# Kernel optimization log

Hardware: AMD Instinct MI355X
Metric: run time of the kernel (lower is better)

Reference implementation:

```python
import jax, jax.numpy as jnp
import numpy as np

B, T, D_MODEL, NHEAD, D_HEAD = 8, 4096, 1024, 16, 64


def setup_inputs() -> dict:
    key = jax.random.key(0)
    ks = jax.random.split(key, 8)
    return {
        "inputs": jax.random.normal(ks[0], (B, T, D_MODEL), jnp.float32),
        "z0": jax.random.normal(ks[1], (NHEAD, D_HEAD), jnp.float32),
        "W_in": jax.random.normal(ks[2], (D_MODEL, D_MODEL), jnp.float32) / np.sqrt(D_MODEL),
        "b_in": jax.random.normal(ks[3], (D_MODEL,), jnp.float32) * 0.01,
        "W_out": jax.random.normal(ks[4], (D_MODEL, D_MODEL), jnp.float32) / np.sqrt(D_MODEL),
        "b_out": jax.random.normal(ks[5], (D_MODEL,), jnp.float32) * 0.01,
        "smoothing_logit": jax.random.normal(ks[6], (NHEAD, 1), jnp.float32),
        "v0": jax.random.normal(ks[7], (1, 1, NHEAD, D_HEAD), jnp.float32),
    }


def reference(inputs, z0, W_in, b_in, W_out, b_out, smoothing_logit, v0):
    b, t, d = inputs.shape
    nhead, d_head = z0.shape
    # in projection -> (b, t, h, d_head)
    values = (inputs @ W_in + b_in).reshape(b, t, nhead, d_head)
    # prepend learned z0, then temporal differencing -> (b, t, h, d_head)
    z0_b = jnp.broadcast_to(z0[None, None], (b, 1, nhead, d_head))
    values = jnp.concatenate([z0_b, values], axis=1)
    values = values[:, 1:] - values[:, :-1]
    # exponential smoothing recurrence: s_j = a*s_{j-1} + (1-a)*v_j, s_{-1} = v0
    alpha = jax.nn.sigmoid(smoothing_logit)           # (h, 1)
    a = alpha[None]                                   # (1, h, 1) broadcast over batch
    s0 = jnp.broadcast_to(v0[0, 0][None], (b, nhead, d_head))

    def step(s, v):                                   # v: (b, h, d_head)
        s = a * s + (1.0 - a) * v
        return s, s

    _, es_out = jax.lax.scan(step, s0, jnp.swapaxes(values, 0, 1))  # (t, b, h, d)
    es_out = jnp.swapaxes(es_out, 0, 1)               # (b, t, h, d_head)
    # prepend v0 -> length t+1
    v0_b = jnp.broadcast_to(v0, (b, 1, nhead, d_head))
    out = jnp.concatenate([v0_b, es_out], axis=1)     # (b, t+1, h, d_head)
    out = out.reshape(b, t + 1, nhead * d_head)
    return out @ W_out + b_out                        # (b, t+1, d_model)
```

## Files before the change

### kernel.cpp

```cpp
#include <hip/hip_runtime.h>
#include <hip/hip_bf16.h>
#include <stdint.h>

#define DEV static __device__ __forceinline__

typedef __attribute__((ext_vector_type(8))) short bf16x8;
typedef __attribute__((ext_vector_type(4))) float f32x4;
typedef unsigned int u32;

static constexpr int T = 4096;
static constexpr int BATCH = 8;
static constexpr int DM = 1024;
static constexpr int M1 = BATCH * T;
static constexpr int M2 = BATCH * (T + 1);
static constexpr int M2P = 257 * 128;
static constexpr int NCH = 64;
static constexpr int CL = T / NCH;

DEV unsigned short f2bf(float f) {
  union { float f; unsigned u; } v; v.f = f;
  unsigned u = v.u;
  return (unsigned short)((u + 0x7fffu + ((u >> 16) & 1u)) >> 16);
}
DEV float bf2f(unsigned short s) {
  union { unsigned u; float f; } v; v.u = ((unsigned)s) << 16;
  return v.f;
}

DEV void gl_lds16(const unsigned short* g, unsigned short* lds) {
  __builtin_amdgcn_global_load_lds(
      (const __attribute__((address_space(1))) u32*)g,
      (__attribute__((address_space(3))) u32*)lds,
      16, 0, 0);
}

__global__ void k_cvt_x(const float4* __restrict__ x, ushort4* __restrict__ o) {
  int i = blockIdx.x * 256 + threadIdx.x;
  float4 v = x[i];
  ushort4 r;
  r.x = f2bf(v.x); r.y = f2bf(v.y); r.z = f2bf(v.z); r.w = f2bf(v.w);
  o[i] = r;
}

__global__ void k_transpose(const float* __restrict__ w0, const float* __restrict__ w1,
                            unsigned short* __restrict__ t0, unsigned short* __restrict__ t1) {
  __shared__ float tile[32][33];
  const float* src = blockIdx.z ? w1 : w0;
  unsigned short* dst = blockIdx.z ? t1 : t0;
  int bx = blockIdx.x * 32;
  int by = blockIdx.y * 32;
  int tx = threadIdx.x & 31, ty = threadIdx.x >> 5;
#pragma unroll
  for (int r = 0; r < 32; r += 8)
    tile[ty + r][tx] = src[(by + ty + r) * DM + bx + tx];
  __syncthreads();
#pragma unroll
  for (int r = 0; r < 32; r += 8)
    dst[(bx + ty + r) * DM + by + tx] = f2bf(tile[tx][ty + r]);
}

template <int MODE>
__global__ __launch_bounds__(256) void k_gemm(const unsigned short* __restrict__ A16,
                                              const unsigned short* __restrict__ Bt16,
                                              const float* __restrict__ bias,
                                              unsigned short* __restrict__ outb,
                                              float* __restrict__ outf, int Mvalid) {
  __shared__ unsigned short sA[128 * 32];
  __shared__ unsigned short sB[128 * 32];

  const int tid = threadIdx.x;
  const int w = tid >> 6, l = tid & 63;

  const int nwg = gridDim.x;
  const int cpx = nwg >> 3;
  const int orig = blockIdx.x;
  const int wg = (orig & 7) * cpx + (orig >> 3);
  const int bm = wg >> 3, bn = wg & 7;
  const int blockM = bm * 128;
  const int blockN = bn * 128;
  const int wr = (w >> 1) * 64, wc = (w & 1) * 64;

  f32x4 acc[4][4];
#pragma unroll
  for (int m = 0; m < 4; m++)
#pragma unroll
    for (int n = 0; n < 4; n++) acc[m][n] = (f32x4){0.f, 0.f, 0.f, 0.f};

  const int srow0 = tid >> 2;
  const int sslot = tid & 3;

  auto stage = [&](int kt) {
    const int k0 = kt * 32;
#pragma unroll
    for (int c = 0; c < 2; c++) {
      const int row = c * 64 + srow0;
      const unsigned short* gA = A16 + (size_t)(blockM + row) * DM + k0 + sslot * 8;
      const unsigned short* gB = Bt16 + (size_t)(blockN + row) * DM + k0 + sslot * 8;
      unsigned short* lA = sA + c * 2048 + w * 512;
      unsigned short* lB = sB + c * 2048 + w * 512;
      gl_lds16(gA, lA);
      gl_lds16(gB, lB);
    }
  };

  const int kg = l >> 4;
  const int rr = l & 15;

  stage(0);
  __syncthreads();

  for (int kt = 0; kt < 32; ++kt) {
    bf16x8 af[4], bfr[4];
#pragma unroll
    for (int m = 0; m < 4; m++)
      af[m] = *(const bf16x8*)(sA + (wr + m * 16 + rr) * 32 + kg * 8);
#pragma unroll
    for (int n = 0; n < 4; n++)
      bfr[n] = *(const bf16x8*)(sB + (wc + n * 16 + rr) * 32 + kg * 8);
#pragma unroll
    for (int m = 0; m < 4; m++)
#pragma unroll
      for (int n = 0; n < 4; n++)
        acc[m][n] = __builtin_amdgcn_mfma_f32_16x16x32_bf16(af[m], bfr[n], acc[m][n], 0, 0, 0);
    __syncthreads();
    if (kt + 1 < 32) {
      stage(kt + 1);
      __syncthreads();
    }
  }

#pragma unroll
  for (int m = 0; m < 4; m++) {
    int row = blockM + wr + m * 16 + (l >> 4) * 4;
#pragma unroll
    for (int n = 0; n < 4; n++) {
      int col = blockN + wc + n * 16 + (l & 15);
      float bv = bias[col];
#pragma unroll
      for (int j = 0; j < 4; j++) {
        float v = acc[m][n][j] + bv;
        if (MODE == 0) {
          outb[(size_t)(row + j) * DM + col] = f2bf(v);
        } else {
          if (row + j < Mvalid) outf[(size_t)(row + j) * DM + col] = v;
        }
      }
    }
  }
}

__global__ void k_scan_partial(const unsigned short* __restrict__ proj,
                               const float* __restrict__ logit,
                               const float* __restrict__ z0,
                               float* __restrict__ chunkend) {
  int b = blockIdx.x >> 6, c = blockIdx.x & 63;
  int ch = threadIdx.x;
  float a = 1.f / (1.f + expf(-logit[ch >> 6]));
  int t0 = c * CL;
  const unsigned short* p = proj + (size_t)(b * T + t0) * DM + ch;
  float pprev = (t0 == 0) ? z0[ch] : bf2f(p[-DM]);
  float s = 0.f;
  for (int j = 0; j < CL; j++) {
    float pv = bf2f(p[(size_t)j * DM]);
    s = a * s + (1.f - a) * (pv - pprev);
    pprev = pv;
  }
  chunkend[(b * NCH + c) * DM + ch] = s;
}

__global__ void k_scan_combine(const float* __restrict__ chunkend,
                               const float* __restrict__ logit,
                               const float* __restrict__ v0,
                               float* __restrict__ enter) {
  int b = blockIdx.x;
  int ch = threadIdx.x;
  float a = 1.f / (1.f + expf(-logit[ch >> 6]));
  float a2 = a * a, a4 = a2 * a2, a8 = a4 * a4, a16 = a8 * a8, a32 = a16 * a16;
  float aL = a32 * a32;
  float e = v0[ch];
  enter[(b * NCH + 0) * DM + ch] = e;
  for (int c = 1; c < NCH; c++) {
    e = aL * e + chunkend[(b * NCH + c - 1) * DM + ch];
    enter[(b * NCH + c) * DM + ch] = e;
  }
}

__global__ void k_scan_final(const unsigned short* __restrict__ proj,
                             const float* __restrict__ logit,
                             const float* __restrict__ z0,
                             const float* __restrict__ v0,
                             const float* __restrict__ enter,
                             unsigned short* __restrict__ S) {
  int b = blockIdx.x >> 6, c = blockIdx.x & 63;
  int ch = threadIdx.x;
  float a = 1.f / (1.f + expf(-logit[ch >> 6]));
  int t0 = c * CL;
  const unsigned short* p = proj + (size_t)(b * T + t0) * DM + ch;
  unsigned short* so = S + (size_t)(b * (T + 1) + t0 + 1) * DM + ch;
  float pprev = (t0 == 0) ? z0[ch] : bf2f(p[-DM]);
  float s = enter[(b * NCH + c) * DM + ch];
  if (c == 0) S[(size_t)b * (T + 1) * DM + ch] = f2bf(v0[ch]);
  for (int j = 0; j < CL; j++) {
    float pv = bf2f(p[(size_t)j * DM]);
    s = a * s + (1.f - a) * (pv - pprev);
    pprev = pv;
    so[(size_t)j * DM] = f2bf(s);
  }
}

__global__ void k_pad(unsigned short* __restrict__ S) {
  int i = blockIdx.x * 256 + threadIdx.x;
  S[(size_t)M2 * DM + i] = 0;
}

extern "C" void kernel_launch(void* const* d_in, const int* in_sizes, int n_in,
                              void* d_out, int out_size, void* d_ws, size_t ws_size,
                              hipStream_t stream) {
  const float* inputs = (const float*)d_in[0];
  const float* z0     = (const float*)d_in[1];
  const float* W_in   = (const float*)d_in[2];
  const float* b_in   = (const float*)d_in[3];
  const float* W_out  = (const float*)d_in[4];
  const float* b_out  = (const float*)d_in[5];
  const float* slogit = (const float*)d_in[6];
  const float* v0     = (const float*)d_in[7];
  float* out = (float*)d_out;

  char* ws = (char*)d_ws;
  unsigned short* X16   = (unsigned short*)(ws);
  unsigned short* P16   = (unsigned short*)(ws + 67108864);
  unsigned short* S16   = (unsigned short*)(ws + 134217728);
  unsigned short* WTin  = (unsigned short*)(ws + 201588736);
  unsigned short* WTout = (unsigned short*)(ws + 203685888);
  float* chunkend       = (float*)(ws + 205783040);
  float* enter          = (float*)(ws + 207880192);

  k_cvt_x<<<32768, 256, 0, stream>>>((const float4*)inputs, (ushort4*)X16);
  k_transpose<<<dim3(32, 32, 2), 256, 0, stream>>>(W_in, W_out, WTin, WTout);
  k_gemm<0><<<dim3((M1 / 128) * 8), 256, 0, stream>>>(X16, WTin, b_in, P16, nullptr, M1);
  k_scan_partial<<<dim3(BATCH * NCH), 1024, 0, stream>>>(P16, slogit, z0, chunkend);
  k_scan_combine<<<dim3(BATCH), 1024, 0, stream>>>(chunkend, slogit, v0, enter);
  k_scan_final<<<dim3(BATCH * NCH), 1024, 0, stream>>>(P16, slogit, z0, v0, enter, S16);
  k_pad<<<dim3(480), 256, 0, stream>>>(S16);
  k_gemm<1><<<dim3((M2P / 128) * 8), 256, 0, stream>>>(S16, WTout, b_out, nullptr, out, M2);
}
```

Before: 315.3 us.

## Rewrite GEMM with 256x256 tiles, 4-stage async LDS pipeline and swizzle

```diff
diff --git a/kernel.cpp b/kernel.cpp
--- a/kernel.cpp
+++ b/kernel.cpp
@@ -13,9 +13,10 @@
 static constexpr int DM = 1024;
 static constexpr int M1 = BATCH * T;
 static constexpr int M2 = BATCH * (T + 1);
-static constexpr int M2P = 257 * 128;
+static constexpr int M2P = 129 * 256;
 static constexpr int NCH = 64;
 static constexpr int CL = T / NCH;
+static constexpr int NT = 32;
 
 DEV unsigned short f2bf(float f) {
   union { float f; unsigned u; } v; v.f = f;
@@ -60,85 +61,116 @@
 }
 
 template <int MODE>
-__global__ __launch_bounds__(256) void k_gemm(const unsigned short* __restrict__ A16,
-                                              const unsigned short* __restrict__ Bt16,
-                                              const float* __restrict__ bias,
-                                              unsigned short* __restrict__ outb,
-                                              float* __restrict__ outf, int Mvalid) {
-  __shared__ unsigned short sA[128 * 32];
-  __shared__ unsigned short sB[128 * 32];
+__global__ __launch_bounds__(512, 2) void k_gemm(const unsigned short* __restrict__ A16,
+                                                 const unsigned short* __restrict__ Bt16,
+                                                 const float* __restrict__ bias,
+                                                 unsigned short* __restrict__ outb,
+                                                 float* __restrict__ outf, int Mvalid) {
+  __shared__ unsigned short lds[4 * 16384];
 
   const int tid = threadIdx.x;
   const int w = tid >> 6, l = tid & 63;
-
-  const int nwg = gridDim.x;
-  const int cpx = nwg >> 3;
-  const int orig = blockIdx.x;
-  const int wg = (orig & 7) * cpx + (orig >> 3);
-  const int bm = wg >> 3, bn = wg & 7;
-  const int blockM = bm * 128;
-  const int blockN = bn * 128;
-  const int wr = (w >> 1) * 64, wc = (w & 1) * 64;
-
-  f32x4 acc[4][4];
-#pragma unroll
-  for (int m = 0; m < 4; m++)
+  const int wm = w >> 2, wn = w & 3;
+  const int rr = l & 15, kg = l >> 4;
+
+  const int nwg = gridDim.x, orig = blockIdx.x;
+  const int q = nwg >> 3, r8 = nwg & 7;
+  const int xcd = orig & 7, idx = orig >> 3;
+  const int wg = (xcd < r8 ? xcd * (q + 1) : r8 * (q + 1) + (xcd - r8) * q) + idx;
+  const int bm = wg >> 2, bn = wg & 3;
+  const int blockM = bm * 256;
+  const int blockN = bn * 256;
+
+  f32x4 acc[8][4];
+#pragma unroll
+  for (int m = 0; m < 8; m++)
 #pragma unroll
     for (int n = 0; n < 4; n++) acc[m][n] = (f32x4){0.f, 0.f, 0.f, 0.f};
 
-  const int srow0 = tid >> 2;
-  const int sslot = tid & 3;
-
-  auto stage = [&](int kt) {
-    const int k0 = kt * 32;
-#pragma unroll
-    for (int c = 0; c < 2; c++) {
-      const int row = c * 64 + srow0;
-      const unsigned short* gA = A16 + (size_t)(blockM + row) * DM + k0 + sslot * 8;
-      const unsigned short* gB = Bt16 + (size_t)(blockN + row) * DM + k0 + sslot * 8;
-      unsigned short* lA = sA + c * 2048 + w * 512;
-      unsigned short* lB = sB + c * 2048 + w * 512;
-      gl_lds16(gA, lA);
-      gl_lds16(gB, lB);
-    }
+  const unsigned short* pA[2];
+  const unsigned short* pB[2];
+#pragma unroll
+  for (int cc = 0; cc < 2; cc++) {
+    int rp = w * 32 + cc * 16 + (l >> 2);
+    int sl = (l & 3) ^ ((rp >> 1) & 3);
+    pA[cc] = A16 + (size_t)(blockM + rp) * DM + sl * 8;
+    pB[cc] = Bt16 + (size_t)(blockN + rp) * DM + sl * 8;
+  }
+
+  int offA[8], offB[4];
+#pragma unroll
+  for (int mf = 0; mf < 8; mf++) {
+    int rrow = wm * 128 + mf * 16 + rr;
+    offA[mf] = rrow * 32 + ((kg ^ ((rrow >> 1) & 3)) * 8);
+  }
+#pragma unroll
+  for (int nf = 0; nf < 4; nf++) {
+    int rb = wn * 64 + nf * 16 + rr;
+    offB[nf] = 8192 + rb * 32 + ((kg ^ ((rb >> 1) & 3)) * 8);
+  }
+
+  auto stageA = [&](int t) {
+    unsigned short* d = lds + (t & 3) * 16384 + w * 1024;
+#pragma unroll
+    for (int cc = 0; cc < 2; cc++) gl_lds16(pA[cc] + (size_t)t * 32, d + cc * 512);
   };
-
-  const int kg = l >> 4;
-  const int rr = l & 15;
-
-  stage(0);
-  __syncthreads();
-
-  for (int kt = 0; kt < 32; ++kt) {
-    bf16x8 af[4], bfr[4];
-#pragma unroll
-    for (int m = 0; m < 4; m++)
-      af[m] = *(const bf16x8*)(sA + (wr + m * 16 + rr) * 32 + kg * 8);
-#pragma unroll
-    for (int n = 0; n < 4; n++)
-      bfr[n] = *(const bf16x8*)(sB + (wc + n * 16 + rr) * 32 + kg * 8);
-#pragma unroll
-    for (int m = 0; m < 4; m++)
-#pragma unroll
-      for (int n = 0; n < 4; n++)
-        acc[m][n] = __builtin_amdgcn_mfma_f32_16x16x32_bf16(af[m], bfr[n], acc[m][n], 0, 0, 0);
-    __syncthreads();
-    if (kt + 1 < 32) {
-      stage(kt + 1);
-      __syncthreads();
-    }
-  }
-
-#pragma unroll
-  for (int m = 0; m < 4; m++) {
-    int row = blockM + wr + m * 16 + (l >> 4) * 4;
-#pragma unroll
-    for (int n = 0; n < 4; n++) {
-      int col = blockN + wc + n * 16 + (l & 15);
-      float bv = bias[col];
+  auto stageB = [&](int t) {
+    unsigned short* d = lds + (t & 3) * 16384 + 8192 + w * 1024;
+#pragma unroll
+    for (int cc = 0; cc < 2; cc++) gl_lds16(pB[cc] + (size_t)t * 32, d + cc * 512);
+  };
+
+  stageA(0); stageB(0);
+  stageA(1); stageB(1);
+  stageA(2); stageB(2);
+
+  for (int t = 0; t < NT; ++t) {
+    if (t < NT - 2)       asm volatile("s_waitcnt vmcnt(8)" ::: "memory");
+    else if (t == NT - 2) asm volatile("s_waitcnt vmcnt(4)" ::: "memory");
+    else                  asm volatile("s_waitcnt vmcnt(0)" ::: "memory");
+    __builtin_amdgcn_s_barrier();
+    asm volatile("" ::: "memory");
+
+    const unsigned short* buf = lds + (t & 3) * 16384;
+    const bool do_stage = (t + 3 < NT);
+
+    bf16x8 bq[4], aq[4];
+#pragma unroll
+    for (int nf = 0; nf < 4; nf++) bq[nf] = *(const bf16x8*)(buf + offB[nf]);
+#pragma unroll
+    for (int mf = 0; mf < 4; mf++) aq[mf] = *(const bf16x8*)(buf + offA[mf]);
+    if (do_stage) stageA(t + 3);
+    __builtin_amdgcn_s_setprio(1);
+#pragma unroll
+    for (int mf = 0; mf < 4; mf++)
+#pragma unroll
+      for (int nf = 0; nf < 4; nf++)
+        acc[mf][nf] = __builtin_amdgcn_mfma_f32_16x16x32_bf16(aq[mf], bq[nf], acc[mf][nf], 0, 0, 0);
+    __builtin_amdgcn_s_setprio(0);
+    __builtin_amdgcn_s_barrier();
+
+#pragma unroll
+    for (int mf = 0; mf < 4; mf++) aq[mf] = *(const bf16x8*)(buf + offA[4 + mf]);
+    if (do_stage) stageB(t + 3);
+    __builtin_amdgcn_s_setprio(1);
+#pragma unroll
+    for (int mf = 0; mf < 4; mf++)
+#pragma unroll
+      for (int nf = 0; nf < 4; nf++)
+        acc[4 + mf][nf] = __builtin_amdgcn_mfma_f32_16x16x32_bf16(aq[mf], bq[nf], acc[4 + mf][nf], 0, 0, 0);
+    __builtin_amdgcn_s_setprio(0);
+  }
+
+#pragma unroll
+  for (int nf = 0; nf < 4; nf++) {
+    int col = blockN + wn * 64 + nf * 16 + (l & 15);
+    float bv = bias[col];
+#pragma unroll
+    for (int mf = 0; mf < 8; mf++) {
+      int row = blockM + wm * 128 + mf * 16 + (l >> 4) * 4;
 #pragma unroll
       for (int j = 0; j < 4; j++) {
-        float v = acc[m][n][j] + bv;
+        float v = acc[mf][nf][j] + bv;
         if (MODE == 0) {
           outb[(size_t)(row + j) * DM + col] = f2bf(v);
         } else {
@@ -210,7 +242,7 @@
 
 __global__ void k_pad(unsigned short* __restrict__ S) {
   int i = blockIdx.x * 256 + threadIdx.x;
-  S[(size_t)M2 * DM + i] = 0;
+  if (i < (M2P - M2) * DM) S[(size_t)M2 * DM + i] = 0;
 }
 
 extern "C" void kernel_launch(void* const* d_in, const int* in_sizes, int n_in,
@@ -230,17 +262,17 @@
   unsigned short* X16   = (unsigned short*)(ws);
   unsigned short* P16   = (unsigned short*)(ws + 67108864);
   unsigned short* S16   = (unsigned short*)(ws + 134217728);
-  unsigned short* WTin  = (unsigned short*)(ws + 201588736);
-  unsigned short* WTout = (unsigned short*)(ws + 203685888);
-  float* chunkend       = (float*)(ws + 205783040);
-  float* enter          = (float*)(ws + 207880192);
+  unsigned short* WTin  = (unsigned short*)(ws + 201850880);
+  unsigned short* WTout = (unsigned short*)(ws + 203948032);
+  float* chunkend       = (float*)(ws + 206045184);
+  float* enter          = (float*)(ws + 208142336);
 
   k_cvt_x<<<32768, 256, 0, stream>>>((const float4*)inputs, (ushort4*)X16);
   k_transpose<<<dim3(32, 32, 2), 256, 0, stream>>>(W_in, W_out, WTin, WTout);
-  k_gemm<0><<<dim3((M1 / 128) * 8), 256, 0, stream>>>(X16, WTin, b_in, P16, nullptr, M1);
+  k_gemm<0><<<dim3((M1 / 256) * 4), 512, 0, stream>>>(X16, WTin, b_in, P16, nullptr, M1);
   k_scan_partial<<<dim3(BATCH * NCH), 1024, 0, stream>>>(P16, slogit, z0, chunkend);
   k_scan_combine<<<dim3(BATCH), 1024, 0, stream>>>(chunkend, slogit, v0, enter);
   k_scan_final<<<dim3(BATCH * NCH), 1024, 0, stream>>>(P16, slogit, z0, v0, enter, S16);
-  k_pad<<<dim3(480), 256, 0, stream>>>(S16);
-  k_gemm<1><<<dim3((M2P / 128) * 8), 256, 0, stream>>>(S16, WTout, b_out, nullptr, out, M2);
-}
+  k_pad<<<dim3(992), 256, 0, stream>>>(S16);
+  k_gemm<1><<<dim3((M2P / 256) * 4), 512, 0, stream>>>(S16, WTout, b_out, nullptr, out, M2);
+}
```

New measurement: 301.5 us. -4.4%, faster.

## Double-buffer GEMM LDS with swizzled BK=64 tiles and vectorized epilogue

Applied to the files above, without the earlier changes.

```diff
diff --git a/kernel.cpp b/kernel.cpp
--- a/kernel.cpp
+++ b/kernel.cpp
@@ -16,6 +16,7 @@
 static constexpr int M2P = 257 * 128;
 static constexpr int NCH = 64;
 static constexpr int CL = T / NCH;
+static constexpr int NT = 16;
 
 DEV unsigned short f2bf(float f) {
   union { float f; unsigned u; } v; v.f = f;
@@ -60,25 +61,24 @@
 }
 
 template <int MODE>
-__global__ __launch_bounds__(256) void k_gemm(const unsigned short* __restrict__ A16,
-                                              const unsigned short* __restrict__ Bt16,
-                                              const float* __restrict__ bias,
-                                              unsigned short* __restrict__ outb,
-                                              float* __restrict__ outf, int Mvalid) {
-  __shared__ unsigned short sA[128 * 32];
-  __shared__ unsigned short sB[128 * 32];
+__global__ __launch_bounds__(256, 2) void k_gemm(const unsigned short* __restrict__ A16,
+                                                 const unsigned short* __restrict__ Bt16,
+                                                 const float* __restrict__ bias,
+                                                 unsigned short* __restrict__ outb,
+                                                 float* __restrict__ outf, int Mvalid) {
+  __shared__ unsigned short lds[2][2][128 * 64];
 
   const int tid = threadIdx.x;
   const int w = tid >> 6, l = tid & 63;
-
-  const int nwg = gridDim.x;
+  const int wm = w >> 1, wn = w & 1;
+  const int lo = l & 15, hi = l >> 4;
+
+  const int nwg = gridDim.x, orig = blockIdx.x;
   const int cpx = nwg >> 3;
-  const int orig = blockIdx.x;
   const int wg = (orig & 7) * cpx + (orig >> 3);
   const int bm = wg >> 3, bn = wg & 7;
   const int blockM = bm * 128;
   const int blockN = bn * 128;
-  const int wr = (w >> 1) * 64, wc = (w & 1) * 64;
 
   f32x4 acc[4][4];
 #pragma unroll
@@ -86,64 +86,82 @@
 #pragma unroll
     for (int n = 0; n < 4; n++) acc[m][n] = (f32x4){0.f, 0.f, 0.f, 0.f};
 
-  const int srow0 = tid >> 2;
-  const int sslot = tid & 3;
-
-  auto stage = [&](int kt) {
-    const int k0 = kt * 32;
-#pragma unroll
-    for (int c = 0; c < 2; c++) {
-      const int row = c * 64 + srow0;
-      const unsigned short* gA = A16 + (size_t)(blockM + row) * DM + k0 + sslot * 8;
-      const unsigned short* gB = Bt16 + (size_t)(blockN + row) * DM + k0 + sslot * 8;
-      unsigned short* lA = sA + c * 2048 + w * 512;
-      unsigned short* lB = sB + c * 2048 + w * 512;
-      gl_lds16(gA, lA);
-      gl_lds16(gB, lB);
+  const int ssw = (l & 7) ^ ((l >> 3) & 7);
+  const unsigned short* pA[4];
+  const unsigned short* pB[4];
+#pragma unroll
+  for (int c = 0; c < 4; c++) {
+    const int rp = w * 32 + c * 8 + (l >> 3);
+    pA[c] = A16 + (size_t)(blockM + rp) * DM + ssw * 8;
+    pB[c] = Bt16 + (size_t)(blockN + rp) * DM + ssw * 8;
+  }
+
+  auto stage = [&](int tt, int buf) {
+#pragma unroll
+    for (int c = 0; c < 4; c++) {
+      gl_lds16(pA[c] + (size_t)tt * 64, &lds[buf][0][(w * 32 + c * 8) * 64]);
+      gl_lds16(pB[c] + (size_t)tt * 64, &lds[buf][1][(w * 32 + c * 8) * 64]);
     }
   };
 
-  const int kg = l >> 4;
-  const int rr = l & 15;
-
-  stage(0);
+  stage(0, 0);
   __syncthreads();
 
-  for (int kt = 0; kt < 32; ++kt) {
-    bf16x8 af[4], bfr[4];
-#pragma unroll
-    for (int m = 0; m < 4; m++)
-      af[m] = *(const bf16x8*)(sA + (wr + m * 16 + rr) * 32 + kg * 8);
-#pragma unroll
-    for (int n = 0; n < 4; n++)
-      bfr[n] = *(const bf16x8*)(sB + (wc + n * 16 + rr) * 32 + kg * 8);
-#pragma unroll
-    for (int m = 0; m < 4; m++)
-#pragma unroll
-      for (int n = 0; n < 4; n++)
-        acc[m][n] = __builtin_amdgcn_mfma_f32_16x16x32_bf16(af[m], bfr[n], acc[m][n], 0, 0, 0);
+  for (int t = 0; t < NT; ++t) {
+    const int cur = t & 1;
+    if (t + 1 < NT) stage(t + 1, cur ^ 1);
+
+    const unsigned short* La = lds[cur][0];
+    const unsigned short* Lb = lds[cur][1];
+    bf16x8 aq[4][2], bq[4][2];
+#pragma unroll
+    for (int kh = 0; kh < 2; kh++) {
+      const int g = kh * 4 + hi;
+#pragma unroll
+      for (int mf = 0; mf < 4; mf++) {
+        const int r = wm * 64 + mf * 16 + lo;
+        aq[mf][kh] = *(const bf16x8*)(La + r * 64 + (g ^ (r & 7)) * 8);
+      }
+#pragma unroll
+      for (int nf = 0; nf < 4; nf++) {
+        const int r = wn * 64 + nf * 16 + lo;
+        bq[nf][kh] = *(const bf16x8*)(Lb + r * 64 + (g ^ (r & 7)) * 8);
+      }
+    }
+#pragma unroll
+    for (int kh = 0; kh < 2; kh++)
+#pragma unroll
+      for (int mf = 0; mf < 4; mf++)
+#pragma unroll
+        for (int nf = 0; nf < 4; nf++)
+          acc[mf][nf] = __builtin_amdgcn_mfma_f32_16x16x32_bf16(
+              bq[nf][kh], aq[mf][kh], acc[mf][nf], 0, 0, 0);
+
     __syncthreads();
-    if (kt + 1 < 32) {
-      stage(kt + 1);
-      __syncthreads();
-    }
-  }
-
-#pragma unroll
-  for (int m = 0; m < 4; m++) {
-    int row = blockM + wr + m * 16 + (l >> 4) * 4;
-#pragma unroll
-    for (int n = 0; n < 4; n++) {
-      int col = blockN + wc + n * 16 + (l & 15);
-      float bv = bias[col];
-#pragma unroll
-      for (int j = 0; j < 4; j++) {
-        float v = acc[m][n][j] + bv;
-        if (MODE == 0) {
-          outb[(size_t)(row + j) * DM + col] = f2bf(v);
-        } else {
-          if (row + j < Mvalid) outf[(size_t)(row + j) * DM + col] = v;
-        }
+  }
+
+#pragma unroll
+  for (int mf = 0; mf < 4; mf++) {
+    const int row = blockM + wm * 64 + mf * 16 + lo;
+    if (MODE == 1 && row >= Mvalid) continue;
+#pragma unroll
+    for (int nf = 0; nf < 4; nf++) {
+      const int col = blockN + wn * 64 + nf * 16 + hi * 4;
+      const float4 bv = *(const float4*)(bias + col);
+      if (MODE == 0) {
+        ushort4 o;
+        o.x = f2bf(acc[mf][nf][0] + bv.x);
+        o.y = f2bf(acc[mf][nf][1] + bv.y);
+        o.z = f2bf(acc[mf][nf][2] + bv.z);
+        o.w = f2bf(acc[mf][nf][3] + bv.w);
+        *(ushort4*)(outb + (size_t)row * DM + col) = o;
+      } else {
+        float4 o;
+        o.x = acc[mf][nf][0] + bv.x;
+        o.y = acc[mf][nf][1] + bv.y;
+        o.z = acc[mf][nf][2] + bv.z;
+        o.w = acc[mf][nf][3] + bv.w;
+        *(float4*)(outf + (size_t)row * DM + col) = o;
       }
     }
   }
```

Result: faster. 278.9 us (-11.5%).
